# Performance work log

Hardware: AMD Instinct MI355X
Metric: run time of the kernel (lower is better)

Reference implementation:

```python
import jax, jax.numpy as jnp
import numpy as np

B, T, D, H = 2, 2048, 1024, 16
HD = D // H
DFF = 4 * D
EPS = 1e-5


def gelu_tanh(x):
    c = jnp.sqrt(2.0 / jnp.pi).astype(x.dtype)
    return 0.5 * x * (1.0 + jnp.tanh(c * (x + 0.044715 * x ** 3)))


def layernorm(x, scale, shift):
    mean = jnp.mean(x, axis=-1, keepdims=True)
    var = jnp.var(x, axis=-1, keepdims=True)  # unbiased=False
    return (x - mean) / jnp.sqrt(var + EPS) * scale + shift


def setup_inputs() -> dict:
    key = jax.random.key(0)
    ks = jax.random.split(key, 12)
    s = lambda fan_in: 1.0 / np.sqrt(fan_in)
    return {
        "x": jax.random.normal(ks[0], (B, T, D), jnp.float32),
        "wq": jax.random.normal(ks[1], (D, D), jnp.float32) * s(D),
        "wk": jax.random.normal(ks[2], (D, D), jnp.float32) * s(D),
        "wv": jax.random.normal(ks[3], (D, D), jnp.float32) * s(D),
        "wo": jax.random.normal(ks[4], (D, D), jnp.float32) * s(D),
        "bo": jnp.zeros((D,), jnp.float32),
        "ln1_scale": jnp.ones((D,), jnp.float32),
        "ln1_shift": jnp.zeros((D,), jnp.float32),
        "ln2_scale": jnp.ones((D,), jnp.float32),
        "ln2_shift": jnp.zeros((D,), jnp.float32),
        "w1": jax.random.normal(ks[5], (D, DFF), jnp.float32) * s(D),
        "b1": jnp.zeros((DFF,), jnp.float32),
        "w2": jax.random.normal(ks[6], (DFF, D), jnp.float32) * s(DFF),
        "b2": jnp.zeros((D,), jnp.float32),
    }


def reference(x, wq, wk, wv, wo, bo, ln1_scale, ln1_shift, ln2_scale, ln2_shift, w1, b1, w2, b2):
    # pre-LN attention
    h = layernorm(x, ln1_scale, ln1_shift)
    q = (h @ wq).reshape(B, T, H, HD).transpose(0, 2, 1, 3)  # [B,H,T,hd]
    k = (h @ wk).reshape(B, T, H, HD).transpose(0, 2, 1, 3)
    v = (h @ wv).reshape(B, T, H, HD).transpose(0, 2, 1, 3)
    scores = jnp.einsum('bhqd,bhkd->bhqk', q, k) / jnp.sqrt(jnp.float32(HD))
    causal = jnp.tril(jnp.ones((T, T), bool))
    scores = jnp.where(causal, scores, -jnp.inf)
    attn = jax.nn.softmax(scores, axis=-1)
    ctx = jnp.einsum('bhqk,bhkd->bhqd', attn, v)
    ctx = ctx.transpose(0, 2, 1, 3).reshape(B, T, D)
    attn_out = ctx @ wo + bo
    x = x + attn_out  # dropout p=0
    # pre-LN FFN
    h2 = layernorm(x, ln2_scale, ln2_shift)
    ff = gelu_tanh(h2 @ w1 + b1) @ w2 + b2
    return x + ff
```

## Files before the change

kernel.cpp:

```cpp
#include <hip/hip_runtime.h>
#include <hip/hip_bf16.h>
#include <stdint.h>

typedef unsigned short u16;
typedef __attribute__((ext_vector_type(8))) short s16x8;
typedef __attribute__((ext_vector_type(4))) float f32x4;

#define B_   2
#define T_   2048
#define D_   1024
#define H_   16
#define HD_  64
#define DFF_ 4096
#define M_   (B_*T_)

#define SC2F 0.18033688f

__device__ __forceinline__ u16 f2b(float f){
  uint32_t u = __float_as_uint(f);
  u += 0x7FFFu + ((u >> 16) & 1u);
  return (u16)(u >> 16);
}
__device__ __forceinline__ uint32_t pk2(float lo, float hi){
  uint32_t r;
  asm volatile("v_cvt_pk_bf16_f32 %0, %1, %2" : "=v"(r) : "v"(lo), "v"(hi));
  return r;
}

__device__ __forceinline__ void gl_lds16(const void* g, void* l){
  __builtin_amdgcn_global_load_lds((const __attribute__((address_space(1))) void*)g,
                                   (__attribute__((address_space(3))) void*)l, 16, 0, 0);
}

template<int N> __device__ __forceinline__ void waitvm(){
  if constexpr (N == 0)      asm volatile("s_waitcnt vmcnt(0)" ::: "memory");
  else if constexpr (N == 2) asm volatile("s_waitcnt vmcnt(2)" ::: "memory");
  else                       asm volatile("s_waitcnt vmcnt(4)" ::: "memory");
}

__global__ __launch_bounds__(256) void wconv_all(const float* __restrict__ wq,
                                                 const float* __restrict__ wk,
                                                 const float* __restrict__ wv,
                                                 const float* __restrict__ wo,
                                                 const float* __restrict__ w1,
                                                 const float* __restrict__ w2,
                                                 u16* __restrict__ wqkvT, u16* __restrict__ woT,
                                                 u16* __restrict__ w1T,   u16* __restrict__ w2T){
  const int bid = blockIdx.x;
  const float* W; u16* Wt; int K, N, tk, tn;
  if (bid < 1024){
    const int which = bid >> 8, t = bid & 255; tk = t >> 4; tn = t & 15; K = 1024; N = 1024;
    W  = (which == 0) ? wq : (which == 1) ? wk : (which == 2) ? wv : wo;
    Wt = (which == 3) ? woT : wqkvT + (size_t)which * D_ * D_;
  } else if (bid < 2048){
    const int t = bid - 1024; tk = t >> 6; tn = t & 63; K = 1024; N = 4096; W = w1; Wt = w1T;
  } else {
    const int t = bid - 2048; tk = t >> 4; tn = t & 15; K = 4096; N = 1024; W = w2; Wt = w2T;
  }
  const int k0 = tk << 6, n0 = tn << 6;
  __shared__ u16 tile[64][68];
  const int tid = threadIdx.x;
  const int rr = tid >> 4, c4 = (tid & 15) << 2;
  #pragma unroll
  for (int rep = 0; rep < 4; rep++){
    int r = rr + (rep << 4);
    float4 v = *reinterpret_cast<const float4*>(W + (size_t)(k0 + r)*N + n0 + c4);
    tile[r][c4+0] = f2b(v.x); tile[r][c4+1] = f2b(v.y);
    tile[r][c4+2] = f2b(v.z); tile[r][c4+3] = f2b(v.w);
  }
  __syncthreads();
  const int rn = tid >> 2, kb = (tid & 3) << 4;
  u16 tmp[16];
  #pragma unroll
  for (int j = 0; j < 16; j++) tmp[j] = tile[kb + j][rn];
  ushort4* dst = reinterpret_cast<ushort4*>(Wt + (size_t)(n0 + rn)*K + k0 + kb);
  dst[0] = make_ushort4(tmp[0], tmp[1], tmp[2], tmp[3]);
  dst[1] = make_ushort4(tmp[4], tmp[5], tmp[6], tmp[7]);
  dst[2] = make_ushort4(tmp[8], tmp[9], tmp[10], tmp[11]);
  dst[3] = make_ushort4(tmp[12], tmp[13], tmp[14], tmp[15]);
}

__global__ __launch_bounds__(256) void ln_kernel(const float* __restrict__ X,
                                                 const float* __restrict__ sc,
                                                 const float* __restrict__ sh,
                                                 u16* __restrict__ out){
  const int row = blockIdx.x;
  const int tid = threadIdx.x;
  float4 a = reinterpret_cast<const float4*>(X + ((size_t)row << 10))[tid];
  float s = a.x + a.y + a.z + a.w;
  float q = a.x*a.x + a.y*a.y + a.z*a.z + a.w*a.w;
  #pragma unroll
  for (int o = 32; o > 0; o >>= 1){ s += __shfl_xor(s, o); q += __shfl_xor(q, o); }
  __shared__ float red[8];
  const int w = tid >> 6;
  if ((tid & 63) == 0){ red[w] = s; red[4 + w] = q; }
  __syncthreads();
  float S = red[0] + red[1] + red[2] + red[3];
  float Q = red[4] + red[5] + red[6] + red[7];
  float mean = S * (1.0f/1024.0f);
  float var  = Q * (1.0f/1024.0f) - mean*mean;
  float inv = rsqrtf(var + 1e-5f);
  float4 gsc = reinterpret_cast<const float4*>(sc)[tid];
  float4 gsh = reinterpret_cast<const float4*>(sh)[tid];
  ushort4 o4;
  o4.x = f2b((a.x - mean)*inv*gsc.x + gsh.x);
  o4.y = f2b((a.y - mean)*inv*gsc.y + gsh.y);
  o4.z = f2b((a.z - mean)*inv*gsc.z + gsh.z);
  o4.w = f2b((a.w - mean)*inv*gsc.w + gsh.w);
  reinterpret_cast<ushort4*>(out + ((size_t)row << 10))[tid] = o4;
}

__global__ __launch_bounds__(256) void reduce2(const float* __restrict__ p,
                                               const float* __restrict__ bias,
                                               const float* __restrict__ resid,
                                               float* __restrict__ out){
  const size_t idx = ((size_t)blockIdx.x << 8) + threadIdx.x;
  float4 a = reinterpret_cast<const float4*>(p)[idx];
  float4 b = reinterpret_cast<const float4*>(p)[idx + (((size_t)M_*D_) >> 2)];
  float4 r = reinterpret_cast<const float4*>(resid)[idx];
  float4 bb = reinterpret_cast<const float4*>(bias)[threadIdx.x];
  float4 o;
  o.x = a.x + b.x + r.x + bb.x;
  o.y = a.y + b.y + r.y + bb.y;
  o.z = a.z + b.z + r.z + bb.z;
  o.w = a.w + b.w + r.w + bb.w;
  reinterpret_cast<float4*>(out)[idx] = o;
}

__global__ __launch_bounds__(256) void reduce_ln(const float* __restrict__ p,
                                                 const float* __restrict__ bias,
                                                 const float* __restrict__ resid,
                                                 const float* __restrict__ sc,
                                                 const float* __restrict__ sh,
                                                 float* __restrict__ x1,
                                                 u16* __restrict__ h2){
  const int row = blockIdx.x;
  const int tid = threadIdx.x;
  const size_t idx = ((size_t)row << 8) + tid;
  float4 a  = reinterpret_cast<const float4*>(p)[idx];
  float4 b  = reinterpret_cast<const float4*>(p)[idx + (((size_t)M_*D_) >> 2)];
  float4 r  = reinterpret_cast<const float4*>(resid)[idx];
  float4 bb = reinterpret_cast<const float4*>(bias)[tid];
  float4 v;
  v.x = a.x + b.x + r.x + bb.x;
  v.y = a.y + b.y + r.y + bb.y;
  v.z = a.z + b.z + r.z + bb.z;
  v.w = a.w + b.w + r.w + bb.w;
  reinterpret_cast<float4*>(x1)[idx] = v;
  float s = v.x + v.y + v.z + v.w;
  float q = v.x*v.x + v.y*v.y + v.z*v.z + v.w*v.w;
  #pragma unroll
  for (int o = 32; o > 0; o >>= 1){ s += __shfl_xor(s, o); q += __shfl_xor(q, o); }
  __shared__ float red[8];
  const int w = tid >> 6;
  if ((tid & 63) == 0){ red[w] = s; red[4 + w] = q; }
  __syncthreads();
  float S = red[0] + red[1] + red[2] + red[3];
  float Q = red[4] + red[5] + red[6] + red[7];
  float mean = S * (1.0f/1024.0f);
  float var  = Q * (1.0f/1024.0f) - mean*mean;
  float inv = rsqrtf(var + 1e-5f);
  float4 gsc = reinterpret_cast<const float4*>(sc)[tid];
  float4 gsh = reinterpret_cast<const float4*>(sh)[tid];
  ushort4 o4;
  o4.x = f2b((v.x - mean)*inv*gsc.x + gsh.x);
  o4.y = f2b((v.y - mean)*inv*gsc.y + gsh.y);
  o4.z = f2b((v.z - mean)*inv*gsc.z + gsh.z);
  o4.w = f2b((v.w - mean)*inv*gsc.w + gsh.w);
  reinterpret_cast<ushort4*>(h2 + ((size_t)row << 10))[tid] = o4;
}

template<int EPI, int NF>
__global__ __launch_bounds__(512, 2) void gemm8(const u16* __restrict__ A, const u16* __restrict__ Bt,
                                                const float* __restrict__ bias,
                                                void* __restrict__ Cv, int M, int N, int K, int lda){
  constexpr int BROWS = NF * 32;
  __shared__ __align__(16) u16 LA[2][2][128*64];
  __shared__ __align__(16) u16 LB[2][2][BROWS*64];
  const int tid = threadIdx.x;
  const int lane = tid & 63;
  const int w = tid >> 6;
  const int wm = w >> 2, wn = w & 3;
  const int g = lane >> 4, l15 = lane & 15;
  const int bnb = (wn & 1) * (NF * 16);

  const int nx = gridDim.x, ny = gridDim.y;
  const int nwg = nx * ny * gridDim.z;
  const int flat = blockIdx.x + nx * (blockIdx.y + ny * blockIdx.z);
  const int nfid = (flat & 7) * (nwg >> 3) + (flat >> 3);
  const int tn = nfid % nx;
  const int rest = nfid / nx;
  const int tm = rest % ny;
  const int kz = rest / ny;
  const int tn0 = tn * (NF * 64);
  const int tm0 = tm << 8;
  const u16* Az = A  + (size_t)kz * K;
  const u16* Bz = Bt + (size_t)kz * K;

  const int arow0 = tid >> 3,         asl0 = (((tid) & 7) ^ (arow0 & 7)) << 3;
  const int arow1 = (tid + 512) >> 3, asl1 = (((tid + 512) & 7) ^ (arow1 & 7)) << 3;

  f32x4 acc[8][NF];
  #pragma unroll
  for (int i = 0; i < 8; i++)
    #pragma unroll
    for (int j = 0; j < NF; j++) acc[i][j] = (f32x4){0.f,0.f,0.f,0.f};
  s16x8 bf[NF][2];

#define STG_A(db, h, tt) do{                                                        \
    gl_lds16(Az + (size_t)(tm0 + (h)*128 + arow0)*lda + ((tt) << 6) + asl0,         \
             &LA[db][h][tid*8]);                                                    \
    gl_lds16(Az + (size_t)(tm0 + (h)*128 + arow1)*lda + ((tt) << 6) + asl1,         \
             &LA[db][h][(tid + 512)*8]);                                            \
  }while(0)
#define STG_B(db, h, tt) do{                                                        \
    gl_lds16(Bz + (size_t)(tn0 + (h)*BROWS + arow0)*lda + ((tt) << 6) + asl0,       \
             &LB[db][h][tid*8]);                                                    \
    if constexpr (NF == 4){                                                         \
      gl_lds16(Bz + (size_t)(tn0 + (h)*BROWS + arow1)*lda + ((tt) << 6) + asl1,     \
               &LB[db][h][(tid + 512)*8]);                                          \
    }                                                                               \
  }while(0)
#define LDAF(db, mf, kk) (*reinterpret_cast<const s16x8*>(                          \
    &LA[db][wm][((mf)*16 + l15)*64 + ((((kk)*4 + g) ^ (l15 & 7)) << 3)]))
#define LDBF(db, nf, kk) (*reinterpret_cast<const s16x8*>(                          \
    &LB[db][wn >> 1][(bnb + (nf)*16 + l15)*64 + ((((kk)*4 + g) ^ (l15 & 7)) << 3)]))
#define BLOAD(db) do{ _Pragma("unroll")                                             \
    for (int nf = 0; nf < NF; nf++){ bf[nf][0] = LDBF(db, nf, 0);                   \
                                     bf[nf][1] = LDBF(db, nf, 1); } }while(0)
#define PH(db, MFA, MFB, STG, WV) do{                                               \
    s16x8 a00 = LDAF(db, MFA, 0), a01 = LDAF(db, MFA, 1);                           \
    s16x8 a10 = LDAF(db, MFB, 0), a11 = LDAF(db, MFB, 1);                           \
    STG;                                                                            \
    WV;                                                                             \
    __builtin_amdgcn_s_barrier();                                                   \
    __builtin_amdgcn_s_setprio(1);                                                  \
    _Pragma("unroll")                                                               \
    for (int nf = 0; nf < NF; nf++){                                                \
      acc[MFA][nf] = __builtin_amdgcn_mfma_f32_16x16x32_bf16(a00, bf[nf][0], acc[MFA][nf], 0,0,0); \
      acc[MFA][nf] = __builtin_amdgcn_mfma_f32_16x16x32_bf16(a01, bf[nf][1], acc[MFA][nf], 0,0,0); \
      acc[MFB][nf] = __builtin_amdgcn_mfma_f32_16x16x32_bf16(a10, bf[nf][0], acc[MFB][nf], 0,0,0); \
      acc[MFB][nf] = __builtin_amdgcn_mfma_f32_16x16x32_bf16(a11, bf[nf][1], acc[MFB][nf], 0,0,0); \
    }                                                                               \
    __builtin_amdgcn_s_setprio(0);                                                  \
    __builtin_amdgcn_s_barrier();                                                   \
  }while(0)

  const int NT = K >> 6;
  STG_B(0, 0, 0); STG_B(0, 1, 0); STG_A(0, 0, 0); STG_A(0, 1, 0);
  STG_B(1, 0, 1); STG_B(1, 1, 1);
  waitvm<NF>();
  __builtin_amdgcn_s_barrier();

  for (int t = 0; t < NT; t += 2){
    const bool last = (t + 2 >= NT);
    BLOAD(0);
    PH(0, 0, 1, STG_A(1, 0, t + 1), );
    PH(0, 2, 3, STG_A(1, 1, t + 1), );
    PH(0, 4, 5, if (!last) STG_B(0, 0, t + 2), );
    PH(0, 6, 7, if (!last) STG_B(0, 1, t + 2),
                if (last) waitvm<0>(); else waitvm<NF>(););
    BLOAD(1);
    PH(1, 0, 1, if (!last) STG_A(0, 0, t + 2), );
    PH(1, 2, 3, if (!last) STG_A(0, 1, t + 2), );
    PH(1, 4, 5, if (!last) STG_B(1, 0, t + 3), );
    PH(1, 6, 7, if (!last) STG_B(1, 1, t + 3),
                if (last) waitvm<0>(); else waitvm<NF>(););
  }
#undef STG_A
#undef STG_B
#undef LDAF
#undef LDBF
#undef BLOAD
#undef PH

  #pragma unroll
  for (int mf = 0; mf < 8; mf++){
    const int mb = tm0 + wm*128 + mf*16 + (g << 2);
    #pragma unroll
    for (int nf = 0; nf < NF; nf++){
      const int n = tn0 + wn*(NF*16) + nf*16 + l15;
      #pragma unroll
      for (int rr = 0; rr < 4; rr++){
        const int m = mb + rr;
        float v = acc[mf][nf][rr];
        if constexpr (EPI == 0){
          ((float*)Cv)[(size_t)kz*((size_t)M*N) + (size_t)m*N + n] = v;
        } else if constexpr (EPI == 1){
          const int sel = n >> 10, nn = n & 1023;
          const int hh = nn >> 6, d = nn & 63;
          if (sel == 0) v *= SC2F;
          ((u16*)Cv)[(size_t)sel*((size_t)M_*D_) +
                     ((((size_t)(m >> 11)*H_ + hh)*T_ + (m & 2047)) << 6) + d] = f2b(v);
        } else {
          float u = v + bias[n];
          float t2 = 0.7978845608f*(u + 0.044715f*u*u*u);
          float e = __expf(2.0f*t2);
          float th = 1.0f - 2.0f/(e + 1.0f);
          ((u16*)Cv)[(size_t)m*N + n] = f2b(0.5f*u*(1.0f + th));
        }
      }
    }
  }
}

__global__ __launch_bounds__(256) void attn_k(const u16* __restrict__ Qg, const u16* __restrict__ Kg,
                                              const u16* __restrict__ Vg, u16* __restrict__ ctx){
  const int flat = blockIdx.x + (blockIdx.y << 4);
  const int xcd = flat & 7, j_ = flat >> 3;
  const int bh  = ((j_ & 3) << 3) + xcd;
  const int pr_ = j_ >> 2;
  const int tid = threadIdx.x;
  const int lane = tid & 63;
  const int w = tid >> 6;
  const int g = lane >> 4, l15 = lane & 15;

  __shared__ __align__(16) u16 Qs[64*64];
  __shared__ __align__(16) u16 Ks[2][64*64];
  __shared__ __align__(16) u16 Vt[2][64*64];
  __shared__ __align__(16) u16 Pl[4][16*64];

  const size_t hb = (size_t)bh * ((size_t)T_*HD_);
  const u16* Qh = Qg + hb;
  const u16* Kh = Kg + hb;
  const u16* Vh = Vg + hb;
  const int b = bh >> 4, hh = bh & 15;

  const int s_r0 = tid >> 3,        s_c0 = (((tid & 7) ^ (s_r0 & 7)) << 3);
  const int s_r1 = (256+tid) >> 3,  s_c1 = ((((256+tid) & 7) ^ (s_r1 & 7)) << 3);
  const int v_kr = tid >> 2, v_d0 = (tid & 3) << 4;

#define SINK_V(buf, q0, q1, q2, q3) do {                                          \
    u16 vv[16] = {q0.x,q0.y,q0.z,q0.w, q1.x,q1.y,q1.z,q1.w,                       \
                  q2.x,q2.y,q2.z,q2.w, q3.x,q3.y,q3.z,q3.w};                      \
    _Pragma("unroll")                                                             \
    for (int j = 0; j < 16; j++){                                                 \
      int d = v_d0 + j;                                                           \
      Vt[buf][d*64 + ((((v_kr >> 3) ^ (d & 7) ^ ((d >> 4) << 1)) & 7) << 3)       \
              + (v_kr & 7)] = vv[j];                                              \
    }                                                                             \
  } while (0)

  for (int ph = 0; ph < 2; ++ph){
    const int qt = ph ? (31 - pr_) : pr_;

    gl_lds16(Qh + (size_t)(qt*64 + s_r0)*HD_ + s_c0, Qs + tid*8);
    gl_lds16(Qh + (size_t)(qt*64 + s_r1)*HD_ + s_c1, Qs + (256+tid)*8);
    gl_lds16(Kh + (size_t)(s_r0)*HD_ + s_c0, Ks[0] + tid*8);
    gl_lds16(Kh + (size_t)(s_r1)*HD_ + s_c1, Ks[0] + (256+tid)*8);
    {
      const u16* vs = Vh + (size_t)v_kr*HD_ + v_d0;
      ushort4 a0 = *(const ushort4*)(vs + 0);
      ushort4 a1 = *(const ushort4*)(vs + 4);
      ushort4 a2 = *(const ushort4*)(vs + 8);
      ushort4 a3 = *(const ushort4*)(vs + 12);
      SINK_V(0, a0, a1, a2, a3);
    }
    __syncthreads();

    s16x8 qa[2];
    #pragma unroll
    for (int kk = 0; kk < 2; kk++){
      int ra = (w << 4) + l15;
      int slot = (kk << 2) + g;
      qa[kk] = *reinterpret_cast<const s16x8*>(Qs + ra*64 + ((slot ^ (ra & 7)) << 3));
    }

    f32x4 accO[4];
    #pragma unroll
    for (int j = 0; j < 4; j++) accO[j] = (f32x4){0.f,0.f,0.f,0.f};
    float mrow = -1e30f, lrow = 0.f;
    const int qlt = (w << 4) + l15;

    for (int kt = 0; kt <= qt; ++kt){
      const int cur = kt & 1, nxt = cur ^ 1;
      const bool pf = (kt < qt);

      ushort4 p0, p1, p2, p3;
      if (pf){
        gl_lds16(Kh + (size_t)((kt+1)*64 + s_r0)*HD_ + s_c0, Ks[nxt] + tid*8);
        gl_lds16(Kh + (size_t)((kt+1)*64 + s_r1)*HD_ + s_c1, Ks[nxt] + (256+tid)*8);
        const u16* vs = Vh + (size_t)((kt+1)*64 + v_kr)*HD_ + v_d0;
        p0 = *(const ushort4*)(vs + 0);
        p1 = *(const ushort4*)(vs + 4);
        p2 = *(const ushort4*)(vs + 8);
        p3 = *(const ushort4*)(vs + 12);
      }

      f32x4 accS[4];
      #pragma unroll
      for (int j = 0; j < 4; j++) accS[j] = (f32x4){0.f,0.f,0.f,0.f};
      __builtin_amdgcn_s_setprio(1);
      #pragma unroll
      for (int jn = 0; jn < 4; jn++){
        #pragma unroll
        for (int kk = 0; kk < 2; kk++){
          int rb = (jn << 4) + l15;
          int slot = (kk << 2) + g;
          s16x8 kf = *reinterpret_cast<const s16x8*>(Ks[cur] + rb*64 + ((slot ^ (rb & 7)) << 3));
          accS[jn] = __builtin_amdgcn_mfma_f32_16x16x32_bf16(kf, qa[kk], accS[jn], 0, 0, 0);
        }
      }
      __builtin_amdgcn_s_setprio(0);

      float sv[4][4];
      #pragma unroll
      for (int jn = 0; jn < 4; jn++)
        #pragma unroll
        for (int rr = 0; rr < 4; rr++){
          float xv = accS[jn][rr];
          if (kt == qt){
            int kl = (jn << 4) + (g << 2) + rr;
            if (kl > qlt) xv = -1e30f;
          }
          sv[jn][rr] = xv;
        }

      float rmax = sv[0][0];
      #pragma unroll
      for (int jn = 0; jn < 4; jn++)
        #pragma unroll
        for (int rr = 0; rr < 4; rr++) rmax = fmaxf(rmax, sv[jn][rr]);
      rmax = fmaxf(rmax, __shfl_xor(rmax, 16));
      rmax = fmaxf(rmax, __shfl_xor(rmax, 32));

      if (__any(rmax > mrow + 8.0f)){
        float mn = fmaxf(mrow, rmax);
        float sf = exp2f(mrow - mn);
        mrow = mn;
        lrow *= sf;
        #pragma unroll
        for (int rr = 0; rr < 4; rr++){
          float sfr = __shfl(sf, ((lane >> 4) << 2) + rr);
          #pragma unroll
          for (int jn = 0; jn < 4; jn++) accO[jn][rr] *= sfr;
        }
      }

      float tsum = 0.f;
      #pragma unroll
      for (int jn = 0; jn < 4; jn++){
        float pv0 = exp2f(sv[jn][0] - mrow);
        float pv1 = exp2f(sv[jn][1] - mrow);
        float pv2 = exp2f(sv[jn][2] - mrow);
        float pv3 = exp2f(sv[jn][3] - mrow);
        tsum += (pv0 + pv1) + (pv2 + pv3);
        int slot = (jn << 1) | (g >> 1);
        int base = l15*64 + (((slot ^ (l15 & 7)) & 7) << 3) + ((g & 1) << 2);
        uint2 pkd = make_uint2(pk2(pv0, pv1), pk2(pv2, pv3));
        *reinterpret_cast<uint2*>(&Pl[w][base]) = pkd;
      }
      tsum += __shfl_xor(tsum, 16);
      tsum += __shfl_xor(tsum, 32);
      lrow += tsum;

      __builtin_amdgcn_s_setprio(1);
      #pragma unroll
      for (int kk = 0; kk < 2; kk++){
        int slot = (kk << 2) + g;
        s16x8 pa = *reinterpret_cast<const s16x8*>(
            &Pl[w][l15*64 + (((slot ^ (l15 & 7)) & 7) << 3)]);
        #pragma unroll
        for (int jn = 0; jn < 4; jn++){
          int vd = (jn << 4) + l15;
          s16x8 vbf = *reinterpret_cast<const s16x8*>(
              Vt[cur] + vd*64 + (((slot ^ (vd & 7) ^ ((vd >> 4) << 1)) & 7) << 3));
          accO[jn] = __builtin_amdgcn_mfma_f32_16x16x32_bf16(pa, vbf, accO[jn], 0, 0, 0);
        }
      }
      __builtin_amdgcn_s_setprio(0);

      if (pf) SINK_V(nxt, p0, p1, p2, p3);
      __syncthreads();
    }

    #pragma unroll
    for (int rr = 0; rr < 4; rr++){
      float lr = __shfl(lrow, ((lane >> 4) << 2) + rr);
      float inv = 1.0f / lr;
      int qrow = qt*64 + (w << 4) + (g << 2) + rr;
      size_t rowbase = ((size_t)(b*T_ + qrow) << 10) + ((size_t)hh << 6);
      #pragma unroll
      for (int jn = 0; jn < 4; jn++){
        int d = (jn << 4) + l15;
        ctx[rowbase + d] = f2b(accO[jn][rr] * inv);
      }
    }
  }
#undef SINK_V
}

extern "C" void kernel_launch(void* const* d_in, const int* in_sizes, int n_in,
                              void* d_out, int out_size, void* d_ws, size_t ws_size,
                              hipStream_t stream){
  (void)in_sizes; (void)n_in; (void)out_size; (void)ws_size;
  const float* x    = (const float*)d_in[0];
  const float* wq   = (const float*)d_in[1];
  const float* wk   = (const float*)d_in[2];
  const float* wv   = (const float*)d_in[3];
  const float* wo   = (const float*)d_in[4];
  const float* bo   = (const float*)d_in[5];
  const float* ln1s = (const float*)d_in[6];
  const float* ln1b = (const float*)d_in[7];
  const float* ln2s = (const float*)d_in[8];
  const float* ln2b = (const float*)d_in[9];
  const float* w1   = (const float*)d_in[10];
  const float* b1   = (const float*)d_in[11];
  const float* w2   = (const float*)d_in[12];
  const float* b2   = (const float*)d_in[13];
  float* out = (float*)d_out;

  char* p = (char*)d_ws;
  u16*  wqkvT = (u16*)p;  p += (size_t)3*D_*D_*2;
  u16*  woT   = (u16*)p;  p += (size_t)D_*D_*2;
  u16*  w1T   = (u16*)p;  p += (size_t)D_*DFF_*2;
  u16*  w2T   = (u16*)p;  p += (size_t)DFF_*D_*2;
  u16*  h     = (u16*)p;  p += (size_t)M_*D_*2;
  u16*  qb    = (u16*)p;  p += (size_t)M_*D_*2;
  u16*  kb    = (u16*)p;  p += (size_t)M_*D_*2;
  u16*  vb    = (u16*)p;  p += (size_t)M_*D_*2;
  u16*  ctx   = (u16*)p;  p += (size_t)M_*D_*2;
  float* x1   = (float*)p; p += (size_t)M_*D_*4;
  u16*  h2    = (u16*)p;  p += (size_t)M_*D_*2;
  u16*  ff1   = (u16*)p;  p += (size_t)M_*DFF_*2;
  (void)kb; (void)vb;
  float* part = (float*)h;

  dim3 blk(256), blk8(512);
  wconv_all<<<3072, blk, 0, stream>>>(wq, wk, wv, wo, w1, w2, wqkvT, woT, w1T, w2T);
  ln_kernel<<<M_, blk, 0, stream>>>(x, ln1s, ln1b, h);
  gemm8<1,4><<<dim3(12,16,1), blk8, 0, stream>>>(h, wqkvT, nullptr, qb, M_, 3*D_, D_, D_);
  attn_k<<<dim3(16,32), blk, 0, stream>>>(qb, qb + (size_t)M_*D_, qb + 2*(size_t)M_*D_, ctx);
  gemm8<0,2><<<dim3(8,16,2), blk8, 0, stream>>>(ctx, woT, nullptr, part, M_, D_, D_/2, D_);
  reduce_ln<<<M_, blk, 0, stream>>>(part, bo, x, ln2s, ln2b, x1, h2);
  gemm8<3,4><<<dim3(16,16,1), blk8, 0, stream>>>(h2, w1T, b1, ff1, M_, DFF_, D_, D_);
  gemm8<0,2><<<dim3(8,16,2), blk8, 0, stream>>>(ff1, w2T, nullptr, part, M_, D_, DFF_/2, DFF_);
  reduce2<<<M_, blk, 0, stream>>>(part, b2, x1, out);
}
```

Measured before the change: 239.5 us.

## Fuse LN1 into weight-convert launch, store split-K partials in bf16, pre-transpose V

```diff
diff --git a/kernel.cpp b/kernel.cpp
--- a/kernel.cpp
+++ b/kernel.cpp
@@ -21,6 +21,7 @@
   u += 0x7FFFu + ((u >> 16) & 1u);
   return (u16)(u >> 16);
 }
+__device__ __forceinline__ float b2f(u16 u){ return __uint_as_float(((uint32_t)u) << 16); }
 __device__ __forceinline__ uint32_t pk2(float lo, float hi){
   uint32_t r;
   asm volatile("v_cvt_pk_bf16_f32 %0, %1, %2" : "=v"(r) : "v"(lo), "v"(hi));
@@ -45,8 +46,39 @@
                                                  const float* __restrict__ w1,
                                                  const float* __restrict__ w2,
                                                  u16* __restrict__ wqkvT, u16* __restrict__ woT,
-                                                 u16* __restrict__ w1T,   u16* __restrict__ w2T){
+                                                 u16* __restrict__ w1T,   u16* __restrict__ w2T,
+                                                 const float* __restrict__ x,
+                                                 const float* __restrict__ ln1s,
+                                                 const float* __restrict__ ln1b,
+                                                 u16* __restrict__ hout){
   const int bid = blockIdx.x;
+  const int tid = threadIdx.x;
+  if (bid >= 3072){
+    const int row = bid - 3072;
+    float4 a = reinterpret_cast<const float4*>(x + ((size_t)row << 10))[tid];
+    float s = a.x + a.y + a.z + a.w;
+    float q = a.x*a.x + a.y*a.y + a.z*a.z + a.w*a.w;
+    #pragma unroll
+    for (int o = 32; o > 0; o >>= 1){ s += __shfl_xor(s, o); q += __shfl_xor(q, o); }
+    __shared__ float red[8];
+    const int w = tid >> 6;
+    if ((tid & 63) == 0){ red[w] = s; red[4 + w] = q; }
+    __syncthreads();
+    float S = red[0] + red[1] + red[2] + red[3];
+    float Q = red[4] + red[5] + red[6] + red[7];
+    float mean = S * (1.0f/1024.0f);
+    float var  = Q * (1.0f/1024.0f) - mean*mean;
+    float inv = rsqrtf(var + 1e-5f);
+    float4 gsc = reinterpret_cast<const float4*>(ln1s)[tid];
+    float4 gsh = reinterpret_cast<const float4*>(ln1b)[tid];
+    ushort4 o4;
+    o4.x = f2b((a.x - mean)*inv*gsc.x + gsh.x);
+    o4.y = f2b((a.y - mean)*inv*gsc.y + gsh.y);
+    o4.z = f2b((a.z - mean)*inv*gsc.z + gsh.z);
+    o4.w = f2b((a.w - mean)*inv*gsc.w + gsh.w);
+    reinterpret_cast<ushort4*>(hout + ((size_t)row << 10))[tid] = o4;
+    return;
+  }
   const float* W; u16* Wt; int K, N, tk, tn;
   if (bid < 1024){
     const int which = bid >> 8, t = bid & 255; tk = t >> 4; tn = t & 15; K = 1024; N = 1024;
@@ -59,7 +91,6 @@
   }
   const int k0 = tk << 6, n0 = tn << 6;
   __shared__ u16 tile[64][68];
-  const int tid = threadIdx.x;
   const int rr = tid >> 4, c4 = (tid & 15) << 2;
   #pragma unroll
   for (int rep = 0; rep < 4; rep++){
@@ -80,54 +111,24 @@
   dst[3] = make_ushort4(tmp[12], tmp[13], tmp[14], tmp[15]);
 }
 
-__global__ __launch_bounds__(256) void ln_kernel(const float* __restrict__ X,
-                                                 const float* __restrict__ sc,
-                                                 const float* __restrict__ sh,
-                                                 u16* __restrict__ out){
-  const int row = blockIdx.x;
-  const int tid = threadIdx.x;
-  float4 a = reinterpret_cast<const float4*>(X + ((size_t)row << 10))[tid];
-  float s = a.x + a.y + a.z + a.w;
-  float q = a.x*a.x + a.y*a.y + a.z*a.z + a.w*a.w;
-  #pragma unroll
-  for (int o = 32; o > 0; o >>= 1){ s += __shfl_xor(s, o); q += __shfl_xor(q, o); }
-  __shared__ float red[8];
-  const int w = tid >> 6;
-  if ((tid & 63) == 0){ red[w] = s; red[4 + w] = q; }
-  __syncthreads();
-  float S = red[0] + red[1] + red[2] + red[3];
-  float Q = red[4] + red[5] + red[6] + red[7];
-  float mean = S * (1.0f/1024.0f);
-  float var  = Q * (1.0f/1024.0f) - mean*mean;
-  float inv = rsqrtf(var + 1e-5f);
-  float4 gsc = reinterpret_cast<const float4*>(sc)[tid];
-  float4 gsh = reinterpret_cast<const float4*>(sh)[tid];
-  ushort4 o4;
-  o4.x = f2b((a.x - mean)*inv*gsc.x + gsh.x);
-  o4.y = f2b((a.y - mean)*inv*gsc.y + gsh.y);
-  o4.z = f2b((a.z - mean)*inv*gsc.z + gsh.z);
-  o4.w = f2b((a.w - mean)*inv*gsc.w + gsh.w);
-  reinterpret_cast<ushort4*>(out + ((size_t)row << 10))[tid] = o4;
-}
-
-__global__ __launch_bounds__(256) void reduce2(const float* __restrict__ p,
+__global__ __launch_bounds__(256) void reduce2(const u16* __restrict__ p,
                                                const float* __restrict__ bias,
                                                const float* __restrict__ resid,
                                                float* __restrict__ out){
   const size_t idx = ((size_t)blockIdx.x << 8) + threadIdx.x;
-  float4 a = reinterpret_cast<const float4*>(p)[idx];
-  float4 b = reinterpret_cast<const float4*>(p)[idx + (((size_t)M_*D_) >> 2)];
+  ushort4 a4 = reinterpret_cast<const ushort4*>(p)[idx];
+  ushort4 b4 = reinterpret_cast<const ushort4*>(p)[idx + (((size_t)M_*D_) >> 2)];
   float4 r = reinterpret_cast<const float4*>(resid)[idx];
   float4 bb = reinterpret_cast<const float4*>(bias)[threadIdx.x];
   float4 o;
-  o.x = a.x + b.x + r.x + bb.x;
-  o.y = a.y + b.y + r.y + bb.y;
-  o.z = a.z + b.z + r.z + bb.z;
-  o.w = a.w + b.w + r.w + bb.w;
+  o.x = b2f(a4.x) + b2f(b4.x) + r.x + bb.x;
+  o.y = b2f(a4.y) + b2f(b4.y) + r.y + bb.y;
+  o.z = b2f(a4.z) + b2f(b4.z) + r.z + bb.z;
+  o.w = b2f(a4.w) + b2f(b4.w) + r.w + bb.w;
   reinterpret_cast<float4*>(out)[idx] = o;
 }
 
-__global__ __launch_bounds__(256) void reduce_ln(const float* __restrict__ p,
+__global__ __launch_bounds__(256) void reduce_ln(const u16* __restrict__ p,
                                                  const float* __restrict__ bias,
                                                  const float* __restrict__ resid,
                                                  const float* __restrict__ sc,
@@ -137,15 +138,15 @@
   const int row = blockIdx.x;
   const int tid = threadIdx.x;
   const size_t idx = ((size_t)row << 8) + tid;
-  float4 a  = reinterpret_cast<const float4*>(p)[idx];
-  float4 b  = reinterpret_cast<const float4*>(p)[idx + (((size_t)M_*D_) >> 2)];
+  ushort4 a4 = reinterpret_cast<const ushort4*>(p)[idx];
+  ushort4 b4 = reinterpret_cast<const ushort4*>(p)[idx + (((size_t)M_*D_) >> 2)];
   float4 r  = reinterpret_cast<const float4*>(resid)[idx];
   float4 bb = reinterpret_cast<const float4*>(bias)[tid];
   float4 v;
-  v.x = a.x + b.x + r.x + bb.x;
-  v.y = a.y + b.y + r.y + bb.y;
-  v.z = a.z + b.z + r.z + bb.z;
-  v.w = a.w + b.w + r.w + bb.w;
+  v.x = b2f(a4.x) + b2f(b4.x) + r.x + bb.x;
+  v.y = b2f(a4.y) + b2f(b4.y) + r.y + bb.y;
+  v.z = b2f(a4.z) + b2f(b4.z) + r.z + bb.z;
+  v.w = b2f(a4.w) + b2f(b4.w) + r.w + bb.w;
   reinterpret_cast<float4*>(x1)[idx] = v;
   float s = v.x + v.y + v.z + v.w;
   float q = v.x*v.x + v.y*v.y + v.z*v.z + v.w*v.w;
@@ -285,13 +286,18 @@
         const int m = mb + rr;
         float v = acc[mf][nf][rr];
         if constexpr (EPI == 0){
-          ((float*)Cv)[(size_t)kz*((size_t)M*N) + (size_t)m*N + n] = v;
+          ((u16*)Cv)[(size_t)kz*((size_t)M*N) + (size_t)m*N + n] = f2b(v);
         } else if constexpr (EPI == 1){
           const int sel = n >> 10, nn = n & 1023;
           const int hh = nn >> 6, d = nn & 63;
+          const int bq = m >> 11, t = m & 2047;
           if (sel == 0) v *= SC2F;
-          ((u16*)Cv)[(size_t)sel*((size_t)M_*D_) +
-                     ((((size_t)(m >> 11)*H_ + hh)*T_ + (m & 2047)) << 6) + d] = f2b(v);
+          size_t dst;
+          if (sel == 2)
+            dst = 2*(size_t)M_*D_ + ((((size_t)(bq*H_ + hh))*HD_ + d) << 11) + t;
+          else
+            dst = (size_t)sel*((size_t)M_*D_) + ((((size_t)bq*H_ + hh)*T_ + t) << 6) + d;
+          ((u16*)Cv)[dst] = f2b(v);
         } else {
           float u = v + bias[n];
           float t2 = 0.7978845608f*(u + 0.044715f*u*u*u);
@@ -328,18 +334,6 @@
 
   const int s_r0 = tid >> 3,        s_c0 = (((tid & 7) ^ (s_r0 & 7)) << 3);
   const int s_r1 = (256+tid) >> 3,  s_c1 = ((((256+tid) & 7) ^ (s_r1 & 7)) << 3);
-  const int v_kr = tid >> 2, v_d0 = (tid & 3) << 4;
-
-#define SINK_V(buf, q0, q1, q2, q3) do {                                          \
-    u16 vv[16] = {q0.x,q0.y,q0.z,q0.w, q1.x,q1.y,q1.z,q1.w,                       \
-                  q2.x,q2.y,q2.z,q2.w, q3.x,q3.y,q3.z,q3.w};                      \
-    _Pragma("unroll")                                                             \
-    for (int j = 0; j < 16; j++){                                                 \
-      int d = v_d0 + j;                                                           \
-      Vt[buf][d*64 + ((((v_kr >> 3) ^ (d & 7) ^ ((d >> 4) << 1)) & 7) << 3)       \
-              + (v_kr & 7)] = vv[j];                                              \
-    }                                                                             \
-  } while (0)
 
   for (int ph = 0; ph < 2; ++ph){
     const int qt = ph ? (31 - pr_) : pr_;
@@ -348,14 +342,8 @@
     gl_lds16(Qh + (size_t)(qt*64 + s_r1)*HD_ + s_c1, Qs + (256+tid)*8);
     gl_lds16(Kh + (size_t)(s_r0)*HD_ + s_c0, Ks[0] + tid*8);
     gl_lds16(Kh + (size_t)(s_r1)*HD_ + s_c1, Ks[0] + (256+tid)*8);
-    {
-      const u16* vs = Vh + (size_t)v_kr*HD_ + v_d0;
-      ushort4 a0 = *(const ushort4*)(vs + 0);
-      ushort4 a1 = *(const ushort4*)(vs + 4);
-      ushort4 a2 = *(const ushort4*)(vs + 8);
-      ushort4 a3 = *(const ushort4*)(vs + 12);
-      SINK_V(0, a0, a1, a2, a3);
-    }
+    gl_lds16(Vh + (size_t)s_r0*T_ + s_c0, Vt[0] + tid*8);
+    gl_lds16(Vh + (size_t)s_r1*T_ + s_c1, Vt[0] + (256+tid)*8);
     __syncthreads();
 
     s16x8 qa[2];
@@ -376,15 +364,11 @@
       const int cur = kt & 1, nxt = cur ^ 1;
       const bool pf = (kt < qt);
 
-      ushort4 p0, p1, p2, p3;
       if (pf){
         gl_lds16(Kh + (size_t)((kt+1)*64 + s_r0)*HD_ + s_c0, Ks[nxt] + tid*8);
         gl_lds16(Kh + (size_t)((kt+1)*64 + s_r1)*HD_ + s_c1, Ks[nxt] + (256+tid)*8);
-        const u16* vs = Vh + (size_t)((kt+1)*64 + v_kr)*HD_ + v_d0;
-        p0 = *(const ushort4*)(vs + 0);
-        p1 = *(const ushort4*)(vs + 4);
-        p2 = *(const ushort4*)(vs + 8);
-        p3 = *(const ushort4*)(vs + 12);
+        gl_lds16(Vh + (size_t)s_r0*T_ + (kt+1)*64 + s_c0, Vt[nxt] + tid*8);
+        gl_lds16(Vh + (size_t)s_r1*T_ + (kt+1)*64 + s_c1, Vt[nxt] + (256+tid)*8);
       }
 
       f32x4 accS[4];
@@ -464,13 +448,12 @@
         for (int jn = 0; jn < 4; jn++){
           int vd = (jn << 4) + l15;
           s16x8 vbf = *reinterpret_cast<const s16x8*>(
-              Vt[cur] + vd*64 + (((slot ^ (vd & 7) ^ ((vd >> 4) << 1)) & 7) << 3));
+              Vt[cur] + vd*64 + (((slot ^ (vd & 7)) & 7) << 3));
           accO[jn] = __builtin_amdgcn_mfma_f32_16x16x32_bf16(pa, vbf, accO[jn], 0, 0, 0);
         }
       }
       __builtin_amdgcn_s_setprio(0);
 
-      if (pf) SINK_V(nxt, p0, p1, p2, p3);
       __syncthreads();
     }
 
@@ -487,7 +470,6 @@
       }
     }
   }
-#undef SINK_V
 }
 
 extern "C" void kernel_launch(void* const* d_in, const int* in_sizes, int n_in,
@@ -524,11 +506,11 @@
   u16*  h2    = (u16*)p;  p += (size_t)M_*D_*2;
   u16*  ff1   = (u16*)p;  p += (size_t)M_*DFF_*2;
   (void)kb; (void)vb;
-  float* part = (float*)h;
+  u16* part = h;
 
   dim3 blk(256), blk8(512);
-  wconv_all<<<3072, blk, 0, stream>>>(wq, wk, wv, wo, w1, w2, wqkvT, woT, w1T, w2T);
-  ln_kernel<<<M_, blk, 0, stream>>>(x, ln1s, ln1b, h);
+  wconv_all<<<3072 + M_, blk, 0, stream>>>(wq, wk, wv, wo, w1, w2, wqkvT, woT, w1T, w2T,
+                                           x, ln1s, ln1b, h);
   gemm8<1,4><<<dim3(12,16,1), blk8, 0, stream>>>(h, wqkvT, nullptr, qb, M_, 3*D_, D_, D_);
   attn_k<<<dim3(16,32), blk, 0, stream>>>(qb, qb + (size_t)M_*D_, qb + 2*(size_t)M_*D_, ctx);
   gemm8<0,2><<<dim3(8,16,2), blk8, 0, stream>>>(ctx, woT, nullptr, part, M_, D_, D_/2, D_);
```

Result: slower. 248.1 us (+3.6%).
